# Performance work log

Hardware: AMD Instinct MI355X
Metric: run time of the kernel (lower is better)

Reference implementation:

```python
import jax, jax.numpy as jnp
import numpy as np

D_MODEL = 1024
NUM_HEADS = 16
HEAD_DIM = D_MODEL // NUM_HEADS
B, S = 4, 2048


def setup_inputs() -> dict:
    key = jax.random.key(0)
    ks = jax.random.split(key, 11)
    sc = 1.0 / np.sqrt(D_MODEL)
    return {
        "query": jax.random.normal(ks[0], (B, S, D_MODEL), jnp.float32),
        "key": jax.random.normal(ks[1], (B, S, D_MODEL), jnp.float32),
        "value": jax.random.normal(ks[2], (B, S, D_MODEL), jnp.float32),
        "Wq": jax.random.normal(ks[3], (D_MODEL, D_MODEL), jnp.float32) * sc,
        "bq": jnp.zeros((D_MODEL,), jnp.float32),
        "Wk": jax.random.normal(ks[4], (D_MODEL, D_MODEL), jnp.float32) * sc,
        "bk": jnp.zeros((D_MODEL,), jnp.float32),
        "Wv": jax.random.normal(ks[5], (D_MODEL, D_MODEL), jnp.float32) * sc,
        "bv": jnp.zeros((D_MODEL,), jnp.float32),
        "Wo": jax.random.normal(ks[6], (D_MODEL, D_MODEL), jnp.float32) * sc,
        "bo": jnp.zeros((D_MODEL,), jnp.float32),
    }


def _split_heads(x):
    b, s, _ = x.shape
    return x.reshape(b, s, NUM_HEADS, HEAD_DIM).transpose(0, 2, 1, 3)  # [B,H,S,Dh]


def reference(query, key, value, Wq, bq, Wk, bk, Wv, bv, Wo, bo):
    q = _split_heads(query @ Wq + bq)
    k = _split_heads(key @ Wk + bk)
    v = _split_heads(value @ Wv + bv)
    scores = jnp.einsum("bhqd,bhkd->bhqk", q, k) / np.sqrt(HEAD_DIM)
    attn = jax.nn.softmax(scores, axis=-1)
    out = jnp.einsum("bhqk,bhkd->bhqd", attn, v)
    out = out.transpose(0, 2, 1, 3).reshape(query.shape[0], -1, D_MODEL)
    return out @ Wo + bo
```

## Files before the change

### kernel.cpp

```cpp
#include <hip/hip_runtime.h>

typedef unsigned short u16;
typedef unsigned int   u32;
typedef unsigned long long u64;
typedef __attribute__((ext_vector_type(8))) short bf16x8;
typedef __attribute__((ext_vector_type(4))) float f32x4;

#define S_  2048
#define DH  64
#define DM  1024
#define BS  8192
#define CS  0.18033688011112042f

static __device__ __forceinline__ float bf2f(u16 v){ return __uint_as_float(((u32)v)<<16); }
static __device__ __forceinline__ u16 f2bf(float f){
  u32 x = __float_as_uint(f);
  return (u16)((x + 0x7fffu + ((x>>16)&1u)) >> 16);
}
#if __has_builtin(__builtin_amdgcn_cvt_pk_bf16_f32)
static __device__ __forceinline__ u32 pk2(float x, float y){
  typedef __attribute__((ext_vector_type(2))) __bf16 bf2v;
  union { bf2v v; u32 u; } c; c.v = __builtin_amdgcn_cvt_pk_bf16_f32(x, y); return c.u;
}
#else
static __device__ __forceinline__ u32 pk2(float x, float y){
  return (u32)f2bf(x) | ((u32)f2bf(y) << 16);
}
#endif
#if __has_builtin(__builtin_amdgcn_exp2f)
#define EXP2F(x) __builtin_amdgcn_exp2f(x)
#else
#define EXP2F(x) exp2f(x)
#endif

static __device__ __forceinline__ void dma16(const u16* g, const u16* l){
  __builtin_amdgcn_global_load_lds(
      (const __attribute__((address_space(1))) u32*)(u64)(uintptr_t)g,
      (__attribute__((address_space(3))) u32*)(u32)(u64)(uintptr_t)l, 16, 0, 0);
}

static __device__ __forceinline__ bf16x8 frag16v(const u16* p){
  union { bf16x8 f; uint4 u; } w;
  w.u = *(const uint4*)p;
  return w.f;
}

__global__ __launch_bounds__(256) void prep(
    const void* __restrict__ w0, const void* __restrict__ w1,
    const void* __restrict__ w2, const void* __restrict__ w3,
    u16* t0, u16* t1, u16* t2, u16* t3, const int f32f){
  __shared__ u16 tile[32][33];
  int z = blockIdx.z;
  int tid = threadIdx.x;
  bool f32 = f32f != 0;
  const void* in = z==0?w0 : z==1?w1 : z==2?w2 : w3;
  u16* out = z==0?t0 : z==1?t1 : z==2?t2 : t3;
  int tx = tid & 31, ty = tid >> 5;
  int c  = blockIdx.x*32 + tx;
  int r0 = blockIdx.y*32;
  for (int i=ty;i<32;i+=8){
    long off = (long)(r0+i)*DM + c;
    tile[i][tx] = f32 ? f2bf(((const float*)in)[off]) : ((const u16*)in)[off];
  }
  __syncthreads();
  int rr = r0 + tx, cb = blockIdx.x*32;
  for (int i=ty;i<32;i+=8) out[(long)(cb+i)*DM + rr] = tile[tx][i];
}

template<int AF32>
__global__ __launch_bounds__(256) void gemm_qkv(
    const void* __restrict__ A0, const void* __restrict__ A1, const void* __restrict__ A2,
    const u16* __restrict__ W0, const u16* __restrict__ W1, const u16* __restrict__ W2,
    const void* __restrict__ bv0, const void* __restrict__ bv1, const void* __restrict__ bv2,
    u16* C0, u16* C1, u16* C2, const int f32f){
  __shared__ __align__(16) u16 As[2][128*32];
  __shared__ __align__(16) u16 Bs[2][128*32];
  int z = blockIdx.z;
  const void* A  = z==0?A0 : z==1?A1 : A2;
  const u16* BT  = z==0?W0 : z==1?W1 : W2;
  const void* bias = z==0?bv0 : z==1?bv1 : bv2;
  u16* C = z==0?C0 : z==1?C1 : C2;
  const bool bF32 = (f32f != 0);
  int tid = threadIdx.x;
  int by = blockIdx.x, bx = blockIdx.y;
  int lane = tid & 63, w = tid >> 6;
  int t = lane & 15, q = lane >> 4;
  int wr = w >> 1, wc = w & 1;
  f32x4 acc[4][4];
  #pragma unroll
  for(int i=0;i<4;i++) for(int j=0;j<4;j++) for(int k=0;k<4;k++) acc[i][j][k]=0.f;

  int sl = (lane & 7) ^ (lane >> 3);
  int srow = ((lane >> 3) << 1) + (sl >> 2);
  const u16* gB = BT + ((long)(bx*128 + w*32 + srow)*DM + (sl&3)*8);
  const int lb = w*1024;
  int rdo = ((t>>1)<<6) + (((((t&1)<<2) | q) ^ (t>>1)) << 3);

  const u16* gA16 = nullptr;
  const float* gAf = nullptr;
  u32 woff0 = 0, woff1 = 0;
  if constexpr (AF32){
    int arow = lane >> 1;
    int akk  = (lane & 1) * 16;
    gAf = (const float*)A + ((long)(by*128 + w*32 + arow)*DM + akk);
    int line = arow >> 1;
    int key  = line & 7;
    int sil0 = ((arow & 1) << 2) | ((lane & 1) << 1);
    woff0 = lb + line*64 + (u32)(((sil0    ) ^ key) << 3);
    woff1 = lb + line*64 + (u32)(((sil0 + 1) ^ key) << 3);
  } else {
    gA16 = (const u16*)A + ((long)(by*128 + w*32 + srow)*DM + (sl&3)*8);
  }

  if constexpr (AF32){
    float4 f0 = ((const float4*)gAf)[0];
    float4 f1 = ((const float4*)gAf)[1];
    float4 f2 = ((const float4*)gAf)[2];
    float4 f3 = ((const float4*)gAf)[3];
    *(uint4*)(&As[0][woff0]) = make_uint4(pk2(f0.x,f0.y),pk2(f0.z,f0.w),pk2(f1.x,f1.y),pk2(f1.z,f1.w));
    *(uint4*)(&As[0][woff1]) = make_uint4(pk2(f2.x,f2.y),pk2(f2.z,f2.w),pk2(f3.x,f3.y),pk2(f3.z,f3.w));
  } else {
    dma16(gA16,         &As[0][lb]);
    dma16(gA16 + 16*DM, &As[0][lb + 512]);
  }
  dma16(gB,         &Bs[0][lb]);
  dma16(gB + 16*DM, &Bs[0][lb + 512]);

  for (int k0=0; k0<DM; k0+=32){
    int cur = (k0>>5)&1;
    float4 f0, f1, f2, f3;
    if (k0+32 < DM){
      if constexpr (AF32){
        const float* ga = gAf + (k0+32);
        f0 = ((const float4*)ga)[0];
        f1 = ((const float4*)ga)[1];
        f2 = ((const float4*)ga)[2];
        f3 = ((const float4*)ga)[3];
        dma16(gB + k0+32,         &Bs[cur^1][lb]);
        dma16(gB + k0+32 + 16*DM, &Bs[cur^1][lb + 512]);
        asm volatile("s_waitcnt vmcnt(6)" ::: "memory");
      } else {
        dma16(gA16 + k0+32,         &As[cur^1][lb]);
        dma16(gA16 + k0+32 + 16*DM, &As[cur^1][lb + 512]);
        dma16(gB + k0+32,           &Bs[cur^1][lb]);
        dma16(gB + k0+32 + 16*DM,   &Bs[cur^1][lb + 512]);
        asm volatile("s_waitcnt vmcnt(4)" ::: "memory");
      }
    } else {
      asm volatile("s_waitcnt vmcnt(0)" ::: "memory");
    }
    asm volatile("s_waitcnt lgkmcnt(0)" ::: "memory");
    __builtin_amdgcn_s_barrier();
    bf16x8 af[4], bfr[4];
    const u16* Ar = &As[cur][wr*2048 + rdo];
    const u16* Br = &Bs[cur][wc*2048 + rdo];
    #pragma unroll
    for (int rt=0;rt<4;rt++) af[rt]  = frag16v(Ar + rt*512);
    #pragma unroll
    for (int ct=0;ct<4;ct++) bfr[ct] = frag16v(Br + ct*512);
    #pragma unroll
    for (int rt=0;rt<4;rt++)
      #pragma unroll
      for (int ct=0;ct<4;ct++)
        acc[rt][ct] = __builtin_amdgcn_mfma_f32_16x16x32_bf16(af[rt], bfr[ct], acc[rt][ct], 0,0,0);
    if constexpr (AF32){
      if (k0+32 < DM){
        *(uint4*)(&As[cur^1][woff0]) = make_uint4(pk2(f0.x,f0.y),pk2(f0.z,f0.w),pk2(f1.x,f1.y),pk2(f1.z,f1.w));
        *(uint4*)(&As[cur^1][woff1]) = make_uint4(pk2(f2.x,f2.y),pk2(f2.z,f2.w),pk2(f3.x,f3.y),pk2(f3.z,f3.w));
      }
    }
    __builtin_amdgcn_s_barrier();
  }

  float scale = (z==0) ? CS : 1.0f;
  #pragma unroll
  for (int ct=0;ct<4;ct++){
    int col = bx*128 + wc*64 + ct*16 + t;
    float bvv = bF32 ? ((const float*)bias)[col] : bf2f(((const u16*)bias)[col]);
    #pragma unroll
    for (int rt=0;rt<4;rt++){
      int row0 = by*128 + wr*64 + rt*16 + q*4;
      if (z == 2){
        int bb = row0 >> 11, s = row0 & 2047;
        long vbase = (long)bb*2097152 + (long)col*2048
                   + (s & ~63) + ((rt>>1)<<5) + (q<<3) + ((rt&1)<<2);
        u32 lo = pk2(acc[rt][ct][0]+bvv, acc[rt][ct][1]+bvv);
        u32 hi = pk2(acc[rt][ct][2]+bvv, acc[rt][ct][3]+bvv);
        *(uint2*)(C + vbase) = make_uint2(lo,hi);
      } else {
        #pragma unroll
        for (int r=0;r<4;r++)
          C[(long)(row0+r)*DM + col] = f2bf((acc[rt][ct][r] + bvv)*scale);
      }
    }
  }
}

__global__ __launch_bounds__(256) void gemm_o(const u16* __restrict__ A,
    const u16* __restrict__ BT, const void* __restrict__ bias, void* __restrict__ C,
    const int f32f){
  __shared__ __align__(16) u16 As[2][128*32];
  __shared__ __align__(16) u16 Bs[2][128*32];
  const int f = f32f;
  int tid = threadIdx.x;
  int by = blockIdx.x, bx = blockIdx.y;
  int lane = tid & 63, w = tid >> 6;
  int t = lane & 15, q = lane >> 4;
  int wr = w >> 1, wc = w & 1;
  f32x4 acc[4][4];
  #pragma unroll
  for(int i=0;i<4;i++) for(int j=0;j<4;j++) for(int k=0;k<4;k++) acc[i][j][k]=0.f;

  int sl = (lane & 7) ^ (lane >> 3);
  int srow = ((lane >> 3) << 1) + (sl >> 2);
  const u16* gA = A  + ((long)(by*128 + w*32 + srow)*DM + (sl&3)*8);
  const u16* gB = BT + ((long)(bx*128 + w*32 + srow)*DM + (sl&3)*8);
  const int lb = w*1024;
  int rdo = ((t>>1)<<6) + (((((t&1)<<2) | q) ^ (t>>1)) << 3);
  dma16(gA,         &As[0][lb]);
  dma16(gA + 16*DM, &As[0][lb + 512]);
  dma16(gB,         &Bs[0][lb]);
  dma16(gB + 16*DM, &Bs[0][lb + 512]);
  for (int k0=0; k0<DM; k0+=32){
    int cur = (k0>>5)&1;
    if (k0+32 < DM){
      dma16(gA + k0+32,         &As[cur^1][lb]);
      dma16(gA + k0+32 + 16*DM, &As[cur^1][lb + 512]);
      dma16(gB + k0+32,         &Bs[cur^1][lb]);
      dma16(gB + k0+32 + 16*DM, &Bs[cur^1][lb + 512]);
      asm volatile("s_waitcnt vmcnt(4)" ::: "memory");
    } else {
      asm volatile("s_waitcnt vmcnt(0)" ::: "memory");
    }
    __builtin_amdgcn_s_barrier();
    bf16x8 af[4], bfr[4];
    const u16* Ar = &As[cur][wr*2048 + rdo];
    const u16* Br = &Bs[cur][wc*2048 + rdo];
    #pragma unroll
    for (int rt=0;rt<4;rt++) af[rt]  = frag16v(Ar + rt*512);
    #pragma unroll
    for (int ct=0;ct<4;ct++) bfr[ct] = frag16v(Br + ct*512);
    #pragma unroll
    for (int rt=0;rt<4;rt++)
      #pragma unroll
      for (int ct=0;ct<4;ct++)
        acc[rt][ct] = __builtin_amdgcn_mfma_f32_16x16x32_bf16(af[rt], bfr[ct], acc[rt][ct], 0,0,0);
    __builtin_amdgcn_s_barrier();
  }
  #pragma unroll
  for (int ct=0;ct<4;ct++){
    int col = bx*128 + wc*64 + ct*16 + t;
    float bvv = f ? ((const float*)bias)[col] : bf2f(((const u16*)bias)[col]);
    #pragma unroll
    for (int rt=0;rt<4;rt++){
      int row0 = by*128 + wr*64 + rt*16 + q*4;
      #pragma unroll
      for (int r=0;r<4;r++){
        long idx = (long)(row0+r)*DM + col;
        float v = acc[rt][ct][r] + bvv;
        if (f) ((float*)C)[idx] = v;
        else   ((u16*)C)[idx]  = f2bf(v);
      }
    }
  }
}

__global__ __launch_bounds__(256,4) void attn5(const u16* __restrict__ Q,
    const u16* __restrict__ Kb, const u16* __restrict__ Vt, u16* __restrict__ O){
  __shared__ __align__(16) u16 Ks[2][4096];
  __shared__ __align__(16) u16 Vs[2][4096];
  int tid = threadIdx.x;
  int bid = blockIdx.x;
  int qt = bid >> 6;
  int s6 = bid & 63;
  int bh = (s6 & 7)*8 + (s6 >> 3);
  int b = bh >> 4, h = bh & 15;
  int lane = tid & 63, w = tid >> 6;
  int t = lane & 15, q = lane >> 4;

  const u16* Qbase = Q + ((long)(b*S_ + qt*128 + w*32 + t)*DM + h*DH + q*8);
  bf16x8 qf[2][2];
  qf[0][0] = frag16v(Qbase);
  qf[0][1] = frag16v(Qbase + 32);
  qf[1][0] = frag16v(Qbase + 16*DM);
  qf[1][1] = frag16v(Qbase + 16*DM + 32);

  int r0 = tid >> 3;
  int cb = ((tid & 7) * 16) ^ ((r0 & 7) << 4);
  const char* gK = (const char*)Kb + (((long)(b*S_ + r0)*DM + h*DH) << 1) + cb;
  const char* gV = (const char*)Vt + ((((long)bh << 17) + ((long)r0 << 11)) << 1) + cb;
  const long gK1 = ((long)32*DM) << 1;
  const long gV1 = ((long)32*S_) << 1;
  const int ld0 = w*512, ld1 = 2048 + w*512;

  f32x4 o[2][4];
  #pragma unroll
  for (int i=0;i<2;i++) for (int j=0;j<4;j++) for (int k=0;k<4;k++) o[i][j][k]=0.f;
  f32x4 o4[2];
  #pragma unroll
  for (int i=0;i<2;i++) for (int k=0;k<4;k++) o4[i][k]=0.f;

  union { bf16x8 f; u32 u[4]; } vone;
  { u32 ovv = (t==0) ? 0x3F803F80u : 0u;
    vone.u[0]=ovv; vone.u[1]=ovv; vone.u[2]=ovv; vone.u[3]=ovv; }

  const int xorv = (t & 7) << 4;

  dma16((const u16*)(gK),       &Ks[0][ld0]);
  dma16((const u16*)(gK + gK1), &Ks[0][ld1]);
  dma16((const u16*)(gV),       &Vs[0][ld0]);
  dma16((const u16*)(gV + gV1), &Vs[0][ld1]);

  for (int kt=0; kt<32; kt++){
    int cur = kt & 1;
    if (kt < 31){
      long ko = ((long)(kt+1)*64*DM) << 1;
      long vo = (long)(kt+1) << 7;
      dma16((const u16*)(gK + ko),       &Ks[cur^1][ld0]);
      dma16((const u16*)(gK + ko + gK1), &Ks[cur^1][ld1]);
      dma16((const u16*)(gV + vo),       &Vs[cur^1][ld0]);
      dma16((const u16*)(gV + vo + gV1), &Vs[cur^1][ld1]);
      asm volatile("s_waitcnt vmcnt(4)" ::: "memory");
    } else {
      asm volatile("s_waitcnt vmcnt(0)" ::: "memory");
    }
    __builtin_amdgcn_s_barrier();

    const u16* Kc = Ks[cur];
    const u16* Vc = Vs[cur];

    f32x4 sacc[2][4];
    #pragma unroll
    for (int i=0;i<2;i++) for (int j=0;j<4;j++) for (int k=0;k<4;k++) sacc[i][j][k]=0.f;
    #pragma unroll
    for (int ks=0; ks<2; ks++){
      int off = ((ks*64 + q*16) ^ xorv) >> 1;
      bf16x8 k0 = frag16v(Kc + (t     )*64 + off);
      bf16x8 k1 = frag16v(Kc + (16 + t)*64 + off);
      bf16x8 k2 = frag16v(Kc + (32 + t)*64 + off);
      bf16x8 k3 = frag16v(Kc + (48 + t)*64 + off);
      __builtin_amdgcn_s_setprio(1);
      #pragma unroll
      for (int rt=0; rt<2; rt++){
        sacc[rt][0] = __builtin_amdgcn_mfma_f32_16x16x32_bf16(k0, qf[rt][ks], sacc[rt][0],0,0,0);
        sacc[rt][1] = __builtin_amdgcn_mfma_f32_16x16x32_bf16(k1, qf[rt][ks], sacc[rt][1],0,0,0);
        sacc[rt][2] = __builtin_amdgcn_mfma_f32_16x16x32_bf16(k2, qf[rt][ks], sacc[rt][2],0,0,0);
        sacc[rt][3] = __builtin_amdgcn_mfma_f32_16x16x32_bf16(k3, qf[rt][ks], sacc[rt][3],0,0,0);
      }
      __builtin_amdgcn_s_setprio(0);
    }

    union { bf16x8 f; u32 u[4]; } af[2][2];
    #pragma unroll
    for (int rt=0; rt<2; rt++){
      float ev[4][4];
      #pragma unroll
      for (int c=0; c<4; c++)
        #pragma unroll
        for (int r=0; r<4; r++) ev[c][r] = EXP2F(sacc[rt][c][r]);
      #pragma unroll
      for (int ks=0; ks<2; ks++){
        af[rt][ks].u[0] = pk2(ev[2*ks  ][0], ev[2*ks  ][1]);
        af[rt][ks].u[1] = pk2(ev[2*ks  ][2], ev[2*ks  ][3]);
        af[rt][ks].u[2] = pk2(ev[2*ks+1][0], ev[2*ks+1][1]);
        af[rt][ks].u[3] = pk2(ev[2*ks+1][2], ev[2*ks+1][3]);
      }
    }

    #pragma unroll
    for (int ks=0; ks<2; ks++){
      int off = ((ks*64 + q*16) ^ xorv) >> 1;
      bf16x8 v0 = frag16v(Vc + (t     )*64 + off);
      bf16x8 v1 = frag16v(Vc + (16 + t)*64 + off);
      bf16x8 v2 = frag16v(Vc + (32 + t)*64 + off);
      bf16x8 v3 = frag16v(Vc + (48 + t)*64 + off);
      __builtin_amdgcn_s_setprio(1);
      #pragma unroll
      for (int rt=0; rt<2; rt++){
        o[rt][0] = __builtin_amdgcn_mfma_f32_16x16x32_bf16(af[rt][ks].f, v0, o[rt][0],0,0,0);
        o[rt][1] = __builtin_amdgcn_mfma_f32_16x16x32_bf16(af[rt][ks].f, v1, o[rt][1],0,0,0);
        o[rt][2] = __builtin_amdgcn_mfma_f32_16x16x32_bf16(af[rt][ks].f, v2, o[rt][2],0,0,0);
        o[rt][3] = __builtin_amdgcn_mfma_f32_16x16x32_bf16(af[rt][ks].f, v3, o[rt][3],0,0,0);
        o4[rt]   = __builtin_amdgcn_mfma_f32_16x16x32_bf16(af[rt][ks].f, vone.f, o4[rt],0,0,0);
      }
      __builtin_amdgcn_s_setprio(0);
    }
    __builtin_amdgcn_s_barrier();
  }

  #pragma unroll
  for (int rt=0; rt<2; rt++){
    #pragma unroll
    for (int r=0; r<4; r++){
      float l = __shfl(o4[rt][r], lane & 48);
      float inv = 1.f / l;
      int row = qt*128 + w*32 + rt*16 + q*4 + r;
      #pragma unroll
      for (int ct=0; ct<4; ct++)
        O[(long)(b*S_ + row)*DM + h*DH + ct*16 + t] = f2bf(o[rt][ct][r] * inv);
    }
  }
}

extern "C" void kernel_launch(void* const* d_in, const int* in_sizes, int n_in,
                              void* d_out, int out_size, void* d_ws, size_t ws_size,
                              hipStream_t stream){
  (void)n_in; (void)out_size; (void)ws_size;
  const void* xq = d_in[0];
  const void* xk = d_in[1];
  const void* xv = d_in[2];
  const void* Wq = d_in[3];
  const void* bq = d_in[4];
  const void* Wk = d_in[5];
  const void* bk = d_in[6];
  const void* Wv = d_in[7];
  const void* bv = d_in[8];
  const void* Wo = d_in[9];
  const void* bo = d_in[10];

  const long NT = (long)BS*DM;
  int f32f = 1;
  if (in_sizes && in_sizes[0] == (int)(NT*2)) f32f = 0;

  u16* base = (u16*)((char*)d_ws + 256);
  u16* Qb  = base;
  u16* Kbf = base + NT;
  u16* Vt  = base + 2*NT;
  u16* WqT = base + 3*NT;
  u16* WkT = WqT + (long)DM*DM;
  u16* WvT = WkT + (long)DM*DM;
  u16* WoT = WvT + (long)DM*DM;

  dim3 gb(256,1,1);
  prep<<<dim3(32,32,4), gb, 0, stream>>>(Wq, Wk, Wv, Wo,
      WqT, WkT, WvT, WoT, f32f);

  if (f32f){
    gemm_qkv<1><<<dim3(64,8,3), gb, 0, stream>>>(xq, xk, xv,
        WqT, WkT, WvT, bq, bk, bv, Qb, Kbf, Vt, f32f);
  } else {
    gemm_qkv<0><<<dim3(64,8,3), gb, 0, stream>>>(xq, xk, xv,
        WqT, WkT, WvT, bq, bk, bv, Qb, Kbf, Vt, f32f);
  }

  attn5<<<dim3(1024,1,1), gb, 0, stream>>>(Qb, Kbf, Vt, Qb );

  gemm_o<<<dim3(64,8,1), gb, 0, stream>>>(Qb, WoT, bo, d_out, f32f);
}
```

Before: 385.1 us.

## DMA fp32 A tiles into LDS for QKV GEMM and peel first score MFMA

In the fp32-input QKV projection, the A operand is now copied straight into a double-buffered fp32 LDS tile with asynchronous DMA, using an XOR swizzle. Conversion to bf16 happens when fragments are read from LDS, replacing the old path that loaded into registers, converted, then stored to LDS. This moves the global-load latency onto the async copy pipeline, at the cost of twice the LDS footprint for A and extra conversion work per read. In the attention kernel, the first K-step of the score MFMA uses a zero accumulator constant, so the per-tile zeroing of the score accumulators is no longer needed.

```diff
diff --git a/kernel.cpp b/kernel.cpp
--- a/kernel.cpp
+++ b/kernel.cpp
@@ -73,7 +73,8 @@
     const u16* __restrict__ W0, const u16* __restrict__ W1, const u16* __restrict__ W2,
     const void* __restrict__ bv0, const void* __restrict__ bv1, const void* __restrict__ bv2,
     u16* C0, u16* C1, u16* C2, const int f32f){
-  __shared__ __align__(16) u16 As[2][128*32];
+  constexpr int ABYTES = AF32 ? 32768 : 16384;
+  __shared__ __align__(16) char AsRaw[ABYTES];
   __shared__ __align__(16) u16 Bs[2][128*32];
   int z = blockIdx.z;
   const void* A  = z==0?A0 : z==1?A1 : A2;
@@ -93,83 +94,94 @@
   int sl = (lane & 7) ^ (lane >> 3);
   int srow = ((lane >> 3) << 1) + (sl >> 2);
   const u16* gB = BT + ((long)(bx*128 + w*32 + srow)*DM + (sl&3)*8);
-  const int lb = w*1024;
+  const int lbB = w*1024;
   int rdo = ((t>>1)<<6) + (((((t&1)<<2) | q) ^ (t>>1)) << 3);
 
-  const u16* gA16 = nullptr;
-  const float* gAf = nullptr;
-  u32 woff0 = 0, woff1 = 0;
   if constexpr (AF32){
-    int arow = lane >> 1;
-    int akk  = (lane & 1) * 16;
-    gAf = (const float*)A + ((long)(by*128 + w*32 + arow)*DM + akk);
-    int line = arow >> 1;
-    int key  = line & 7;
-    int sil0 = ((arow & 1) << 2) | ((lane & 1) << 1);
-    woff0 = lb + line*64 + (u32)(((sil0    ) ^ key) << 3);
-    woff1 = lb + line*64 + (u32)(((sil0 + 1) ^ key) << 3);
-  } else {
-    gA16 = (const u16*)A + ((long)(by*128 + w*32 + srow)*DM + (sl&3)*8);
-  }
-
-  if constexpr (AF32){
-    float4 f0 = ((const float4*)gAf)[0];
-    float4 f1 = ((const float4*)gAf)[1];
-    float4 f2 = ((const float4*)gAf)[2];
-    float4 f3 = ((const float4*)gAf)[3];
-    *(uint4*)(&As[0][woff0]) = make_uint4(pk2(f0.x,f0.y),pk2(f0.z,f0.w),pk2(f1.x,f1.y),pk2(f1.z,f1.w));
-    *(uint4*)(&As[0][woff1]) = make_uint4(pk2(f2.x,f2.y),pk2(f2.z,f2.w),pk2(f3.x,f3.y),pk2(f3.z,f3.w));
-  } else {
-    dma16(gA16,         &As[0][lb]);
-    dma16(gA16 + 16*DM, &As[0][lb + 512]);
-  }
-  dma16(gB,         &Bs[0][lb]);
-  dma16(gB + 16*DM, &Bs[0][lb + 512]);
-
-  for (int k0=0; k0<DM; k0+=32){
-    int cur = (k0>>5)&1;
-    float4 f0, f1, f2, f3;
-    if (k0+32 < DM){
-      if constexpr (AF32){
-        const float* ga = gAf + (k0+32);
-        f0 = ((const float4*)ga)[0];
-        f1 = ((const float4*)ga)[1];
-        f2 = ((const float4*)ga)[2];
-        f3 = ((const float4*)ga)[3];
-        dma16(gB + k0+32,         &Bs[cur^1][lb]);
-        dma16(gB + k0+32 + 16*DM, &Bs[cur^1][lb + 512]);
+    float* Af = (float*)AsRaw;
+    const float* gA[4];
+    #pragma unroll
+    for (int i=0;i<4;i++){
+      int arow = i*8 + (lane>>3);
+      int slA  = (lane&7) ^ (arow&7);
+      gA[i] = (const float*)A + ((long)(by*128 + w*32 + arow)*DM + slA*4);
+    }
+    const int lbA = w*1024;
+    const int aro = (t&7);
+
+    #pragma unroll
+    for (int i=0;i<4;i++) dma16((const u16*)gA[i], (const u16*)(Af + lbA + i*256));
+    dma16(gB,         &Bs[0][lbB]);
+    dma16(gB + 16*DM, &Bs[0][lbB + 512]);
+
+    for (int k0=0; k0<DM; k0+=32){
+      int cur = (k0>>5)&1;
+      if (k0+32 < DM){
+        #pragma unroll
+        for (int i=0;i<4;i++)
+          dma16((const u16*)(gA[i] + k0+32), (const u16*)(Af + (cur^1)*4096 + lbA + i*256));
+        dma16(gB + k0+32,         &Bs[cur^1][lbB]);
+        dma16(gB + k0+32 + 16*DM, &Bs[cur^1][lbB + 512]);
         asm volatile("s_waitcnt vmcnt(6)" ::: "memory");
       } else {
-        dma16(gA16 + k0+32,         &As[cur^1][lb]);
-        dma16(gA16 + k0+32 + 16*DM, &As[cur^1][lb + 512]);
-        dma16(gB + k0+32,           &Bs[cur^1][lb]);
-        dma16(gB + k0+32 + 16*DM,   &Bs[cur^1][lb + 512]);
+        asm volatile("s_waitcnt vmcnt(0)" ::: "memory");
+      }
+      __builtin_amdgcn_s_barrier();
+      union { bf16x8 f; u32 u[4]; } af[4];
+      bf16x8 bfr[4];
+      const float* Ac = Af + cur*4096;
+      #pragma unroll
+      for (int rt=0;rt<4;rt++){
+        int R = wr*64 + rt*16 + t;
+        const float* pr = Ac + R*32;
+        float4 x0 = *(const float4*)(pr + (((2*q  ) ^ aro) << 2));
+        float4 x1 = *(const float4*)(pr + (((2*q+1) ^ aro) << 2));
+        af[rt].u[0] = pk2(x0.x,x0.y); af[rt].u[1] = pk2(x0.z,x0.w);
+        af[rt].u[2] = pk2(x1.x,x1.y); af[rt].u[3] = pk2(x1.z,x1.w);
+      }
+      const u16* Br = &Bs[cur][wc*2048 + rdo];
+      #pragma unroll
+      for (int ct=0;ct<4;ct++) bfr[ct] = frag16v(Br + ct*512);
+      #pragma unroll
+      for (int rt=0;rt<4;rt++)
+        #pragma unroll
+        for (int ct=0;ct<4;ct++)
+          acc[rt][ct] = __builtin_amdgcn_mfma_f32_16x16x32_bf16(af[rt].f, bfr[ct], acc[rt][ct], 0,0,0);
+      __builtin_amdgcn_s_barrier();
+    }
+  } else {
+    u16 (*As)[128*32] = (u16(*)[128*32])AsRaw;
+    const u16* gA = (const u16*)A + ((long)(by*128 + w*32 + srow)*DM + (sl&3)*8);
+    dma16(gA,         &As[0][lbB]);
+    dma16(gA + 16*DM, &As[0][lbB + 512]);
+    dma16(gB,         &Bs[0][lbB]);
+    dma16(gB + 16*DM, &Bs[0][lbB + 512]);
+    for (int k0=0; k0<DM; k0+=32){
+      int cur = (k0>>5)&1;
+      if (k0+32 < DM){
+        dma16(gA + k0+32,         &As[cur^1][lbB]);
+        dma16(gA + k0+32 + 16*DM, &As[cur^1][lbB + 512]);
+        dma16(gB + k0+32,         &Bs[cur^1][lbB]);
+        dma16(gB + k0+32 + 16*DM, &Bs[cur^1][lbB + 512]);
         asm volatile("s_waitcnt vmcnt(4)" ::: "memory");
-      }
-    } else {
-      asm volatile("s_waitcnt vmcnt(0)" ::: "memory");
-    }
-    asm volatile("s_waitcnt lgkmcnt(0)" ::: "memory");
-    __builtin_amdgcn_s_barrier();
-    bf16x8 af[4], bfr[4];
-    const u16* Ar = &As[cur][wr*2048 + rdo];
-    const u16* Br = &Bs[cur][wc*2048 + rdo];
-    #pragma unroll
-    for (int rt=0;rt<4;rt++) af[rt]  = frag16v(Ar + rt*512);
-    #pragma unroll
-    for (int ct=0;ct<4;ct++) bfr[ct] = frag16v(Br + ct*512);
-    #pragma unroll
-    for (int rt=0;rt<4;rt++)
-      #pragma unroll
-      for (int ct=0;ct<4;ct++)
-        acc[rt][ct] = __builtin_amdgcn_mfma_f32_16x16x32_bf16(af[rt], bfr[ct], acc[rt][ct], 0,0,0);
-    if constexpr (AF32){
-      if (k0+32 < DM){
-        *(uint4*)(&As[cur^1][woff0]) = make_uint4(pk2(f0.x,f0.y),pk2(f0.z,f0.w),pk2(f1.x,f1.y),pk2(f1.z,f1.w));
-        *(uint4*)(&As[cur^1][woff1]) = make_uint4(pk2(f2.x,f2.y),pk2(f2.z,f2.w),pk2(f3.x,f3.y),pk2(f3.z,f3.w));
-      }
-    }
-    __builtin_amdgcn_s_barrier();
+      } else {
+        asm volatile("s_waitcnt vmcnt(0)" ::: "memory");
+      }
+      __builtin_amdgcn_s_barrier();
+      bf16x8 af[4], bfr[4];
+      const u16* Ar = &As[cur][wr*2048 + rdo];
+      const u16* Br = &Bs[cur][wc*2048 + rdo];
+      #pragma unroll
+      for (int rt=0;rt<4;rt++) af[rt]  = frag16v(Ar + rt*512);
+      #pragma unroll
+      for (int ct=0;ct<4;ct++) bfr[ct] = frag16v(Br + ct*512);
+      #pragma unroll
+      for (int rt=0;rt<4;rt++)
+        #pragma unroll
+        for (int ct=0;ct<4;ct++)
+          acc[rt][ct] = __builtin_amdgcn_mfma_f32_16x16x32_bf16(af[rt], bfr[ct], acc[rt][ct], 0,0,0);
+      __builtin_amdgcn_s_barrier();
+    }
   }
 
   float scale = (z==0) ? CS : 1.0f;
@@ -300,6 +312,8 @@
   #pragma unroll
   for (int i=0;i<2;i++) for (int k=0;k<4;k++) o4[i][k]=0.f;
 
+  const f32x4 z4 = {0.f, 0.f, 0.f, 0.f};
+
   union { bf16x8 f; u32 u[4]; } vone;
   { u32 ovv = (t==0) ? 0x3F803F80u : 0u;
     vone.u[0]=ovv; vone.u[1]=ovv; vone.u[2]=ovv; vone.u[3]=ovv; }
@@ -330,11 +344,8 @@
     const u16* Vc = Vs[cur];
 
     f32x4 sacc[2][4];
-    #pragma unroll
-    for (int i=0;i<2;i++) for (int j=0;j<4;j++) for (int k=0;k<4;k++) sacc[i][j][k]=0.f;
-    #pragma unroll
-    for (int ks=0; ks<2; ks++){
-      int off = ((ks*64 + q*16) ^ xorv) >> 1;
+    {
+      int off = ((q*16) ^ xorv) >> 1;
       bf16x8 k0 = frag16v(Kc + (t     )*64 + off);
       bf16x8 k1 = frag16v(Kc + (16 + t)*64 + off);
       bf16x8 k2 = frag16v(Kc + (32 + t)*64 + off);
@@ -342,10 +353,26 @@
       __builtin_amdgcn_s_setprio(1);
       #pragma unroll
       for (int rt=0; rt<2; rt++){
-        sacc[rt][0] = __builtin_amdgcn_mfma_f32_16x16x32_bf16(k0, qf[rt][ks], sacc[rt][0],0,0,0);
-        sacc[rt][1] = __builtin_amdgcn_mfma_f32_16x16x32_bf16(k1, qf[rt][ks], sacc[rt][1],0,0,0);
-        sacc[rt][2] = __builtin_amdgcn_mfma_f32_16x16x32_bf16(k2, qf[rt][ks], sacc[rt][2],0,0,0);
-        sacc[rt][3] = __builtin_amdgcn_mfma_f32_16x16x32_bf16(k3, qf[rt][ks], sacc[rt][3],0,0,0);
+        sacc[rt][0] = __builtin_amdgcn_mfma_f32_16x16x32_bf16(k0, qf[rt][0], z4, 0,0,0);
+        sacc[rt][1] = __builtin_amdgcn_mfma_f32_16x16x32_bf16(k1, qf[rt][0], z4, 0,0,0);
+        sacc[rt][2] = __builtin_amdgcn_mfma_f32_16x16x32_bf16(k2, qf[rt][0], z4, 0,0,0);
+        sacc[rt][3] = __builtin_amdgcn_mfma_f32_16x16x32_bf16(k3, qf[rt][0], z4, 0,0,0);
+      }
+      __builtin_amdgcn_s_setprio(0);
+    }
+    {
+      int off = ((64 + q*16) ^ xorv) >> 1;
+      bf16x8 k0 = frag16v(Kc + (t     )*64 + off);
+      bf16x8 k1 = frag16v(Kc + (16 + t)*64 + off);
+      bf16x8 k2 = frag16v(Kc + (32 + t)*64 + off);
+      bf16x8 k3 = frag16v(Kc + (48 + t)*64 + off);
+      __builtin_amdgcn_s_setprio(1);
+      #pragma unroll
+      for (int rt=0; rt<2; rt++){
+        sacc[rt][0] = __builtin_amdgcn_mfma_f32_16x16x32_bf16(k0, qf[rt][1], sacc[rt][0],0,0,0);
+        sacc[rt][1] = __builtin_amdgcn_mfma_f32_16x16x32_bf16(k1, qf[rt][1], sacc[rt][1],0,0,0);
+        sacc[rt][2] = __builtin_amdgcn_mfma_f32_16x16x32_bf16(k2, qf[rt][1], sacc[rt][2],0,0,0);
+        sacc[rt][3] = __builtin_amdgcn_mfma_f32_16x16x32_bf16(k3, qf[rt][1], sacc[rt][3],0,0,0);
       }
       __builtin_amdgcn_s_setprio(0);
     }
```

Measured after the change: 393.8 us. 1.02x slower.
